# Performance work log

Hardware: AMD Instinct MI355X
Metric: run time of the kernel (lower is better)

The kernel has to match this reference:

```python
import jax, jax.numpy as jnp
from jax import lax
import numpy as np

B, C_IN, H, W = 32, 128, 64, 64
C_OUT, K, KH, KW = 256, 4, 3, 3
HIDDEN = C_IN  # in_planes != 3 -> hidden_planes = in_planes
T_TEMP = 34.0
BN_EPS = 1e-5


def setup_inputs() -> dict:
    key = jax.random.key(0)
    ks = jax.random.split(key, 4)
    return {
        "x": jax.random.normal(ks[0], (B, C_IN, H, W), dtype=jnp.float32),
        "w_fc1": jax.random.normal(ks[1], (HIDDEN, C_IN), dtype=jnp.float32) * (2.0 / C_IN) ** 0.5,
        "bn1_gamma": jnp.ones((HIDDEN,), jnp.float32),
        "bn1_beta": jnp.zeros((HIDDEN,), jnp.float32),
        "bn1_mean": jnp.zeros((HIDDEN,), jnp.float32),
        "bn1_var": jnp.ones((HIDDEN,), jnp.float32),
        "w_fc2": jax.random.normal(ks[2], (K * C_IN, HIDDEN), dtype=jnp.float32) * (2.0 / HIDDEN) ** 0.5,
        "b_fc2": jnp.zeros((K * C_IN,), jnp.float32),
        "bn2_gamma": jnp.ones((K * C_IN,), jnp.float32),
        "bn2_beta": jnp.zeros((K * C_IN,), jnp.float32),
        "bn2_mean": jnp.zeros((K * C_IN,), jnp.float32),
        "bn2_var": jnp.ones((K * C_IN,), jnp.float32),
        "anchored_w": jax.random.normal(ks[3], (K, C_OUT, C_IN, KH, KW), dtype=jnp.float32) * (2.0 / (C_OUT * KH * KW)) ** 0.5,
        "anchored_b": jnp.zeros((K, C_OUT), jnp.float32),
    }


def _bn(v, gamma, beta, mean, var):
    return (v - mean) * gamma * lax.rsqrt(var + BN_EPS) + beta


def reference(x, w_fc1, bn1_gamma, bn1_beta, bn1_mean, bn1_var,
              w_fc2, b_fc2, bn2_gamma, bn2_beta, bn2_mean, bn2_var,
              anchored_w, anchored_b):
    # ----- CFG routing: squeeze-excite style softmax over K*C_in -----
    pooled = x.mean(axis=(2, 3))                      # [B, C_in]  (adaptive avg pool to 1x1)
    h = pooled @ w_fc1.T                              # [B, hidden] (1x1 conv, no bias)
    h = jax.nn.relu(_bn(h, bn1_gamma, bn1_beta, bn1_mean, bn1_var))
    t = h @ w_fc2.T + b_fc2                           # [B, K*C_in]
    t = _bn(t, bn2_gamma, bn2_beta, bn2_mean, bn2_var)
    theta = jax.nn.softmax(t / T_TEMP, axis=1)        # [B, K*C_in]
    theta_r = theta.reshape(-1, K, anchored_w.shape[2])  # [B, K, C_in]

    # ----- per-sample kernel mixture: sum_k theta[b,k,i] * W[k,o,i,h,w] -----
    w = jnp.einsum('bki,koihw->boihw', theta_r, anchored_w)  # [B, C_out, C_in, KH, KW]
    b = theta_r.mean(axis=2) @ anchored_b                    # [B, C_out]

    # ----- per-sample conv (equiv. to grouped conv with groups=B) -----
    def conv1(xi, wi):
        return lax.conv_general_dilated(
            xi[None], wi, window_strides=(1, 1), padding=((1, 1), (1, 1)),
            dimension_numbers=('NCHW', 'OIHW', 'NCHW'))[0]

    out = jax.vmap(conv1)(x, w) + b[:, :, None, None]  # [B, C_out, H, W]
    return out
```

## Files before the change

### kernel.cpp

```cpp
#include <hip/hip_runtime.h>

typedef __attribute__((ext_vector_type(8))) __bf16 bf16x8;
typedef __attribute__((ext_vector_type(4))) float f32x4;

__device__ __forceinline__ unsigned short f2bf(float f) {
  unsigned u = __builtin_bit_cast(unsigned, f);
  u = (u + 0x7fffu + ((u >> 16) & 1u)) >> 16;
  return (unsigned short)u;
}

__device__ __forceinline__ void gload_lds16(const void* g, void* l) {
  __builtin_amdgcn_global_load_lds(
      (const __attribute__((address_space(1))) unsigned int*)g,
      (__attribute__((address_space(3))) unsigned int*)l, 16, 0, 0);
}

__global__ __launch_bounds__(256) void k_pool_convert(
    const float* __restrict__ x, float* __restrict__ psum,
    unsigned short* __restrict__ xbf) {
  __shared__ float xs[128][65];
  const int b = blockIdx.x >> 6;
  const int y = blockIdx.x & 63;
  const int t = threadIdx.x;
  const float* src = x + ((size_t)b * 128) * 4096 + y * 64;
#pragma unroll
  for (int i = 0; i < 8; ++i) {
    int idx = t + i * 256;
    int c = idx >> 4, x4 = (idx & 15) << 2;
    float4 v = *(const float4*)(src + (size_t)c * 4096 + x4);
    xs[c][x4] = v.x; xs[c][x4 + 1] = v.y; xs[c][x4 + 2] = v.z; xs[c][x4 + 3] = v.w;
  }
  __syncthreads();
  if (t < 128) {
    float s = 0.f;
#pragma unroll
    for (int j = 0; j < 64; ++j) s += xs[t][j];
    psum[((size_t)b * 128 + t) * 64 + y] = s;
  }
#pragma unroll
  for (int i = 0; i < 4; ++i) {
    int idx = t + i * 256;
    int q = idx & 3, xx = (idx >> 2) & 63, g = idx >> 8;
    unsigned wd[4];
#pragma unroll
    for (int j = 0; j < 4; ++j) {
      unsigned lo = f2bf(xs[g * 32 + q * 8 + 2 * j][xx]);
      unsigned hi = f2bf(xs[g * 32 + q * 8 + 2 * j + 1][xx]);
      wd[j] = lo | (hi << 16);
    }
    *(uint4*)(xbf + ((((size_t)b * 4 + g) * 4096) + y * 64 + xx) * 32 + q * 8) =
        make_uint4(wd[0], wd[1], wd[2], wd[3]);
  }
}

__global__ __launch_bounds__(128) void k_route(
    const float* __restrict__ psum, const float* __restrict__ w_fc1,
    const float* __restrict__ g1, const float* __restrict__ be1,
    const float* __restrict__ m1, const float* __restrict__ v1,
    const float* __restrict__ w_fc2, const float* __restrict__ bfc2,
    const float* __restrict__ g2, const float* __restrict__ be2,
    const float* __restrict__ m2, const float* __restrict__ v2,
    const float* __restrict__ ab, float* __restrict__ theta,
    float* __restrict__ bias) {
  __shared__ float pooled[128], hs[128], red[128], tkm[4];
  const int b = blockIdx.x, t = threadIdx.x;
  float s = 0.f;
  const float* ps = psum + ((size_t)b * 128 + t) * 64;
  for (int j = 0; j < 64; ++j) s += ps[j];
  pooled[t] = s * (1.0f / 4096.0f);
  __syncthreads();
  float acc = 0.f;
  const float* w1r = w_fc1 + t * 128;
  for (int i = 0; i < 128; ++i) acc += pooled[i] * w1r[i];
  acc = (acc - m1[t]) * g1[t] * rsqrtf(v1[t] + 1e-5f) + be1[t];
  hs[t] = fmaxf(acc, 0.f);
  __syncthreads();
  float tv[4];
  for (int q = 0; q < 4; ++q) {
    int m = q * 128 + t;
    const float* w2r = w_fc2 + (size_t)m * 128;
    float a2 = bfc2[m];
    for (int i = 0; i < 128; ++i) a2 += hs[i] * w2r[i];
    a2 = (a2 - m2[m]) * g2[m] * rsqrtf(v2[m] + 1e-5f) + be2[m];
    tv[q] = a2 * (1.0f / 34.0f);
  }
  float mx = fmaxf(fmaxf(tv[0], tv[1]), fmaxf(tv[2], tv[3]));
  red[t] = mx; __syncthreads();
  for (int o = 64; o > 0; o >>= 1) { if (t < o) red[t] = fmaxf(red[t], red[t + o]); __syncthreads(); }
  mx = red[0]; __syncthreads();
  float e[4], ssum = 0.f;
  for (int q = 0; q < 4; ++q) { e[q] = expf(tv[q] - mx); ssum += e[q]; }
  red[t] = ssum; __syncthreads();
  for (int o = 64; o > 0; o >>= 1) { if (t < o) red[t] += red[t + o]; __syncthreads(); }
  float inv = 1.0f / red[0]; __syncthreads();
  float th[4];
  for (int q = 0; q < 4; ++q) { th[q] = e[q] * inv; theta[b * 512 + q * 128 + t] = th[q]; }
  for (int q = 0; q < 4; ++q) {
    red[t] = th[q]; __syncthreads();
    for (int o = 64; o > 0; o >>= 1) { if (t < o) red[t] += red[t + o]; __syncthreads(); }
    if (t == 0) tkm[q] = red[0] * (1.0f / 128.0f);
    __syncthreads();
  }
  for (int o = t; o < 256; o += 128) {
    float bb = 0.f;
    for (int k = 0; k < 4; ++k) bb += tkm[k] * ab[k * 256 + o];
    bias[b * 256 + o] = bb;
  }
}

__global__ __launch_bounds__(256) void k_mix(
    const float* __restrict__ aw, const float* __restrict__ theta,
    unsigned short* __restrict__ wmix) {
  __shared__ float aw_s[4][32][33];
  __shared__ float th_s[32][4][32];
  const int bx = blockIdx.x;
  const int oq = bx & 3, obl = (bx >> 2) & 1, ks = bx >> 3;
  const int g = ks / 9, tt = ks % 9;
  const int tid = threadIdx.x;
#pragma unroll
  for (int i = 0; i < 16; ++i) {
    int e = tid + i * 256;
    int i32 = e & 31, o32 = (e >> 5) & 31, k = e >> 10;
    aw_s[k][i32][o32] =
        aw[((size_t)((k * 256 + obl * 128 + oq * 32 + o32) * 128) + g * 32 + i32) * 9 + tt];
    int kb = (e >> 5) & 3, bb = e >> 7;
    th_s[bb][kb][i32] = theta[bb * 512 + kb * 128 + g * 32 + i32];
  }
  __syncthreads();
  for (int it = 0; it < 16; ++it) {
    int b = it * 2 + (tid >> 7);
    int u = tid & 127;
    int o32 = u >> 2, q = u & 3;
    unsigned wd[4];
#pragma unroll
    for (int jj = 0; jj < 4; ++jj) {
      int i0 = q * 8 + jj * 2, i1 = i0 + 1;
      float v0 = th_s[b][0][i0] * aw_s[0][i0][o32] + th_s[b][1][i0] * aw_s[1][i0][o32]
               + th_s[b][2][i0] * aw_s[2][i0][o32] + th_s[b][3][i0] * aw_s[3][i0][o32];
      float v1 = th_s[b][0][i1] * aw_s[0][i1][o32] + th_s[b][1][i1] * aw_s[1][i1][o32]
               + th_s[b][2][i1] * aw_s[2][i1][o32] + th_s[b][3][i1] * aw_s[3][i1][o32];
      wd[jj] = (unsigned)f2bf(v0) | ((unsigned)f2bf(v1) << 16);
    }
    unsigned A = (unsigned)(((oq * 32 + o32) * 32 + q * 8) * 2);
    unsigned P = A ^ ((A >> 2) & 0x70u);
    size_t tilebase = (((size_t)b * 36 + ks) * 2 + obl) * 8192;
    *(uint4*)((char*)wmix + tilebase + P) = make_uint4(wd[0], wd[1], wd[2], wd[3]);
  }
}

__global__ __launch_bounds__(256, 2) void k_conv(
    const unsigned short* __restrict__ xbf, const unsigned short* __restrict__ wmix,
    const float* __restrict__ bias, float* __restrict__ out) {
  __shared__ __align__(16) char xls[21120];
  __shared__ __align__(16) char wls[2][16384];
  const int bx = blockIdx.x;
  const int wgid = ((bx & 7) << 7) | (bx >> 3);
  const int b = wgid >> 5, pblk = wgid & 31;
  const int tid = threadIdx.x;
  const int lane = tid & 63, wv = tid >> 6;
  const int y0 = pblk << 1;
  const int l15 = lane & 15, l4 = lane >> 4;

  unsigned a_off0 = ((unsigned)(l15 * 64 + l4 * 16)) ^ ((unsigned)(l15 & 7) << 4);
  a_off0 += (unsigned)(wv * 4096);

  f32x4 acc[4][8] = {};

  const unsigned short* xsrc_b = xbf + (size_t)b * 4 * 4096 * 32;

  auto stageW = [&](int ks, int buf) {
    const char* wsrc = (const char*)wmix + (size_t)(b * 36 + ks) * 16384;
#pragma unroll
    for (int p = 0; p < 4; ++p)
      gload_lds16(wsrc + p * 4096 + wv * 1024 + lane * 16,
                  wls[buf] + p * 4096 + wv * 1024);
  };

  uint4 xr[5];
  auto loadX = [&](int g) {
    const unsigned short* xsrc = xsrc_b + (size_t)g * (4096 * 32);
#pragma unroll
    for (int i = 0; i < 4; ++i) {
      int e = tid + i * 256;
      int q = e & 3, rc = e >> 2, c = rc % 66, r = rc / 66;
      int yy = y0 - 1 + r, xx = c - 1;
      uint4 v = make_uint4(0u, 0u, 0u, 0u);
      if ((unsigned)yy < 64u && (unsigned)xx < 64u)
        v = *(const uint4*)(xsrc + (((size_t)yy << 6) + xx) * 32 + q * 8);
      xr[i] = v;
    }
    if (tid < 32) {
      int e = tid + 1024;
      int q = e & 3, rc = e >> 2, c = rc % 66, r = rc / 66;
      int yy = y0 - 1 + r, xx = c - 1;
      uint4 v = make_uint4(0u, 0u, 0u, 0u);
      if ((unsigned)yy < 64u && (unsigned)xx < 64u)
        v = *(const uint4*)(xsrc + (((size_t)yy << 6) + xx) * 32 + q * 8);
      xr[4] = v;
    }
  };
  auto writeX = [&]() {
#pragma unroll
    for (int i = 0; i < 4; ++i) {
      int e = tid + i * 256;
      int q = e & 3, rc = e >> 2, c = rc % 66, r = rc / 66;
      *(uint4*)(xls + (r * 66 + c) * 80 + q * 16) = xr[i];
    }
    if (tid < 32) {
      int e = tid + 1024;
      int q = e & 3, rc = e >> 2, c = rc % 66, r = rc / 66;
      *(uint4*)(xls + (r * 66 + c) * 80 + q * 16) = xr[4];
    }
  };

  loadX(0);
  writeX();
  stageW(0, 0);
  asm volatile("s_waitcnt lgkmcnt(0)" ::: "memory");

#pragma unroll
  for (int ks = 0; ks < 36; ++ks) {
    asm volatile("s_waitcnt vmcnt(0)" ::: "memory");
    __builtin_amdgcn_s_barrier();
    asm volatile("" ::: "memory");
    if (ks > 0 && ks % 9 == 0) {
      writeX();
      asm volatile("s_waitcnt lgkmcnt(0)" ::: "memory");
      __builtin_amdgcn_s_barrier();
      asm volatile("" ::: "memory");
    }
    if (ks % 9 == 8 && ks < 35) {
      loadX(ks / 9 + 1);
      asm volatile("" ::: "memory");
    }
    if (ks + 1 < 36) stageW(ks + 1, (ks + 1) & 1);
    const int dy = (ks % 9) / 3, dx = (ks % 9) % 3;
    bf16x8 bfr[8], afr[4];
    const char* bbase = xls + ((0 + dy) * 66 + dx + l15) * 80 + l4 * 16;
#pragma unroll
    for (int pf = 0; pf < 4; ++pf) bfr[pf] = *(const bf16x8*)(bbase + pf * 1280);
#pragma unroll
    for (int pf = 0; pf < 4; ++pf) bfr[pf + 4] = *(const bf16x8*)(bbase + 5280 + pf * 1280);
    const char* abase = wls[ks & 1] + a_off0;
#pragma unroll
    for (int of = 0; of < 4; ++of) afr[of] = *(const bf16x8*)(abase + of * 1024);
    __builtin_amdgcn_s_setprio(1);
#pragma unroll
    for (int of = 0; of < 4; ++of)
#pragma unroll
      for (int pf = 0; pf < 8; ++pf)
        acc[of][pf] = __builtin_amdgcn_mfma_f32_16x16x32_bf16(afr[of], bfr[pf], acc[of][pf], 0, 0, 0);
    __builtin_amdgcn_s_setprio(0);
  }

  const float* bp = bias + b * 256 + wv * 64;
  float bv[4][4];
#pragma unroll
  for (int of = 0; of < 4; ++of)
#pragma unroll
    for (int j = 0; j < 4; ++j) bv[of][j] = bp[of * 16 + l4 * 4 + j];
  size_t outbase = ((size_t)(b * 256 + wv * 64)) * 4096 + (size_t)y0 * 64;
#pragma unroll
  for (int of = 0; of < 4; ++of)
#pragma unroll
    for (int pf = 0; pf < 8; ++pf) {
      int py = pf >> 2, px0 = (pf & 3) * 16;
#pragma unroll
      for (int j = 0; j < 4; ++j)
        out[outbase + (size_t)(of * 16 + l4 * 4 + j) * 4096 + py * 64 + px0 + l15] =
            acc[of][pf][j] + bv[of][j];
    }
}

extern "C" void kernel_launch(void* const* d_in, const int* in_sizes, int n_in,
                              void* d_out, int out_size, void* d_ws, size_t ws_size,
                              hipStream_t stream) {
  const float* x     = (const float*)d_in[0];
  const float* w_fc1 = (const float*)d_in[1];
  const float* g1    = (const float*)d_in[2];
  const float* be1   = (const float*)d_in[3];
  const float* m1    = (const float*)d_in[4];
  const float* v1    = (const float*)d_in[5];
  const float* w_fc2 = (const float*)d_in[6];
  const float* bfc2  = (const float*)d_in[7];
  const float* g2    = (const float*)d_in[8];
  const float* be2   = (const float*)d_in[9];
  const float* m2    = (const float*)d_in[10];
  const float* v2    = (const float*)d_in[11];
  const float* aw    = (const float*)d_in[12];
  const float* ab    = (const float*)d_in[13];
  float* out = (float*)d_out;

  char* ws = (char*)d_ws;
  unsigned short* xbf  = (unsigned short*)(ws);
  unsigned short* wmix = (unsigned short*)(ws + 33554432);
  float* psum  = (float*)(ws + 52428800);
  float* theta = (float*)(ws + 53477376);
  float* bias  = (float*)(ws + 53542912);

  hipLaunchKernelGGL(k_pool_convert, dim3(2048), dim3(256), 0, stream, x, psum, xbf);
  hipLaunchKernelGGL(k_route, dim3(32), dim3(128), 0, stream, psum, w_fc1, g1, be1, m1, v1,
                     w_fc2, bfc2, g2, be2, m2, v2, ab, theta, bias);
  hipLaunchKernelGGL(k_mix, dim3(288), dim3(256), 0, stream, aw, theta, wmix);
  hipLaunchKernelGGL(k_conv, dim3(1024), dim3(256), 0, stream, xbf, wmix, bias, out);
}
```

Measured before the change: 132.6 us.

## Load mixed conv weights directly into registers in fragment order, drop LDS staging

The weight-mixing kernel now writes the per-sample bf16 weights in the exact MFMA A-fragment layout, so each lane of the conv kernel can read its fragments with coalesced 16-byte global loads. The LDS double buffer for weights, the global_load_lds staging and the per-step barriers are removed, leaving synchronization only at the four input-channel group boundaries. Weight fragments are prefetched two steps ahead in registers. This cuts LDS traffic and barrier stalls, but puts global load latency directly on the MFMA path and raises register pressure under the 2-blocks-per-SM launch bound.

```diff
diff --git a/kernel.cpp b/kernel.cpp
--- a/kernel.cpp
+++ b/kernel.cpp
@@ -7,12 +7,6 @@
   unsigned u = __builtin_bit_cast(unsigned, f);
   u = (u + 0x7fffu + ((u >> 16) & 1u)) >> 16;
   return (unsigned short)u;
-}
-
-__device__ __forceinline__ void gload_lds16(const void* g, void* l) {
-  __builtin_amdgcn_global_load_lds(
-      (const __attribute__((address_space(1))) unsigned int*)g,
-      (__attribute__((address_space(3))) unsigned int*)l, 16, 0, 0);
 }
 
 __global__ __launch_bounds__(256) void k_pool_convert(
@@ -141,10 +135,10 @@
                + th_s[b][2][i1] * aw_s[2][i1][o32] + th_s[b][3][i1] * aw_s[3][i1][o32];
       wd[jj] = (unsigned)f2bf(v0) | ((unsigned)f2bf(v1) << 16);
     }
-    unsigned A = (unsigned)(((oq * 32 + o32) * 32 + q * 8) * 2);
-    unsigned P = A ^ ((A >> 2) & 0x70u);
-    size_t tilebase = (((size_t)b * 36 + ks) * 2 + obl) * 8192;
-    *(uint4*)((char*)wmix + tilebase + P) = make_uint4(wd[0], wd[1], wd[2], wd[3]);
+    int o = obl * 128 + oq * 32 + o32;
+    unsigned off = (unsigned)((o >> 6) * 4096 + ((o >> 4) & 3) * 1024 + q * 256 + (o & 15) * 16);
+    size_t tilebase = ((size_t)b * 36 + ks) * 16384;
+    *(uint4*)((char*)wmix + tilebase + off) = make_uint4(wd[0], wd[1], wd[2], wd[3]);
   }
 }
 
@@ -152,7 +146,6 @@
     const unsigned short* __restrict__ xbf, const unsigned short* __restrict__ wmix,
     const float* __restrict__ bias, float* __restrict__ out) {
   __shared__ __align__(16) char xls[21120];
-  __shared__ __align__(16) char wls[2][16384];
   const int bx = blockIdx.x;
   const int wgid = ((bx & 7) << 7) | (bx >> 3);
   const int b = wgid >> 5, pblk = wgid & 31;
@@ -161,20 +154,11 @@
   const int y0 = pblk << 1;
   const int l15 = lane & 15, l4 = lane >> 4;
 
-  unsigned a_off0 = ((unsigned)(l15 * 64 + l4 * 16)) ^ ((unsigned)(l15 & 7) << 4);
-  a_off0 += (unsigned)(wv * 4096);
-
   f32x4 acc[4][8] = {};
 
   const unsigned short* xsrc_b = xbf + (size_t)b * 4 * 4096 * 32;
-
-  auto stageW = [&](int ks, int buf) {
-    const char* wsrc = (const char*)wmix + (size_t)(b * 36 + ks) * 16384;
-#pragma unroll
-    for (int p = 0; p < 4; ++p)
-      gload_lds16(wsrc + p * 4096 + wv * 1024 + lane * 16,
-                  wls[buf] + p * 4096 + wv * 1024);
-  };
+  const char* wtile = (const char*)wmix + (size_t)(b * 36) * 16384 +
+                      (size_t)wv * 4096 + (size_t)lane * 16;
 
   uint4 xr[5];
   auto loadX = [&](int g) {
@@ -215,42 +199,51 @@
 
   loadX(0);
   writeX();
-  stageW(0, 0);
-  asm volatile("s_waitcnt lgkmcnt(0)" ::: "memory");
-
-#pragma unroll
-  for (int ks = 0; ks < 36; ++ks) {
-    asm volatile("s_waitcnt vmcnt(0)" ::: "memory");
-    __builtin_amdgcn_s_barrier();
-    asm volatile("" ::: "memory");
-    if (ks > 0 && ks % 9 == 0) {
+  __syncthreads();
+
+  bf16x8 wf[2][4];
+#pragma unroll
+  for (int of = 0; of < 4; ++of) wf[0][of] = *(const bf16x8*)(wtile + of * 1024);
+#pragma unroll
+  for (int of = 0; of < 4; ++of) wf[1][of] = *(const bf16x8*)(wtile + 16384 + of * 1024);
+
+#pragma unroll
+  for (int g = 0; g < 4; ++g) {
+    if (g > 0) {
+      __syncthreads();
       writeX();
-      asm volatile("s_waitcnt lgkmcnt(0)" ::: "memory");
-      __builtin_amdgcn_s_barrier();
-      asm volatile("" ::: "memory");
-    }
-    if (ks % 9 == 8 && ks < 35) {
-      loadX(ks / 9 + 1);
-      asm volatile("" ::: "memory");
-    }
-    if (ks + 1 < 36) stageW(ks + 1, (ks + 1) & 1);
-    const int dy = (ks % 9) / 3, dx = (ks % 9) % 3;
-    bf16x8 bfr[8], afr[4];
-    const char* bbase = xls + ((0 + dy) * 66 + dx + l15) * 80 + l4 * 16;
-#pragma unroll
-    for (int pf = 0; pf < 4; ++pf) bfr[pf] = *(const bf16x8*)(bbase + pf * 1280);
-#pragma unroll
-    for (int pf = 0; pf < 4; ++pf) bfr[pf + 4] = *(const bf16x8*)(bbase + 5280 + pf * 1280);
-    const char* abase = wls[ks & 1] + a_off0;
-#pragma unroll
-    for (int of = 0; of < 4; ++of) afr[of] = *(const bf16x8*)(abase + of * 1024);
-    __builtin_amdgcn_s_setprio(1);
-#pragma unroll
-    for (int of = 0; of < 4; ++of)
-#pragma unroll
-      for (int pf = 0; pf < 8; ++pf)
-        acc[of][pf] = __builtin_amdgcn_mfma_f32_16x16x32_bf16(afr[of], bfr[pf], acc[of][pf], 0, 0, 0);
-    __builtin_amdgcn_s_setprio(0);
+      __syncthreads();
+    }
+#pragma unroll
+    for (int t = 0; t < 9; ++t) {
+      const int ks = g * 9 + t;
+      const int dy = t / 3, dx = t % 3;
+      bf16x8 bfr[8];
+      const char* bbase = xls + (dy * 66 + dx + l15) * 80 + l4 * 16;
+#pragma unroll
+      for (int pf = 0; pf < 4; ++pf) bfr[pf] = *(const bf16x8*)(bbase + pf * 1280);
+#pragma unroll
+      for (int pf = 0; pf < 4; ++pf) bfr[pf + 4] = *(const bf16x8*)(bbase + 5280 + pf * 1280);
+      if (t == 8 && g < 3) loadX(g + 1);
+      bf16x8 wN[4];
+      if (ks + 2 < 36) {
+#pragma unroll
+        for (int of = 0; of < 4; ++of)
+          wN[of] = *(const bf16x8*)(wtile + (size_t)(ks + 2) * 16384 + of * 1024);
+      }
+      __builtin_amdgcn_s_setprio(1);
+#pragma unroll
+      for (int of = 0; of < 4; ++of)
+#pragma unroll
+        for (int pf = 0; pf < 8; ++pf)
+          acc[of][pf] = __builtin_amdgcn_mfma_f32_16x16x32_bf16(wf[ks & 1][of], bfr[pf],
+                                                                acc[of][pf], 0, 0, 0);
+      __builtin_amdgcn_s_setprio(0);
+      if (ks + 2 < 36) {
+#pragma unroll
+        for (int of = 0; of < 4; ++of) wf[ks & 1][of] = wN[of];
+      }
+    }
   }
 
   const float* bp = bias + b * 256 + wv * 64;
```

After: 148.4 us. +11.9%, slower.
